# Kernel optimization log

Hardware: AMD Instinct MI355X
Metric: run time of the kernel (lower is better)

The kernel has to match this reference:

```python
import jax, jax.numpy as jnp
import numpy as np
import math

ROPE_BASE = 10000.0
ALIBI_SLOPE = 2.0 ** (-8.0)  # _get_alibi_slopes(1) == [2**(-8*1/1)]


def _rope_cos_sin(T, d):
    inv_freq = 1.0 / (ROPE_BASE ** (jnp.arange(0, d, 2, dtype=jnp.float32) / d))
    t = jnp.arange(T, dtype=jnp.float32)
    freqs = jnp.einsum('i,j->ij', t, inv_freq)          # [T, d/2]
    emb = jnp.concatenate([freqs, freqs], axis=-1)      # [T, d]
    return jnp.cos(emb), jnp.sin(emb)


def _rotate_half(x):
    x1, x2 = jnp.split(x, 2, axis=-1)
    return jnp.concatenate([-x2, x1], axis=-1)


def setup_inputs() -> dict:
    key = jax.random.key(0)
    kq, kk, kv = jax.random.split(key, 3)
    B, T, H = 8, 2048, 256
    return {
        'q': jax.random.normal(kq, (B, T, H), dtype=jnp.float32),
        'k': jax.random.normal(kk, (B, T, H), dtype=jnp.float32),
        'v': jax.random.normal(kv, (B, T, H), dtype=jnp.float32),
    }


def reference(q, k, v):
    B, T, H = q.shape  # num_heads == 1, so head_dim == H
    cos, sin = _rope_cos_sin(T, H)                      # [T, H]
    qe = q * cos + _rotate_half(q) * sin                # [B, T, H]
    ke = k * cos + _rotate_half(k) * sin                # [B, T, H]

    scale = 1.0 / math.sqrt(H)
    scores = jnp.einsum('btd,bsd->bts', qe, ke) * scale  # [B, T, T]

    pos = jnp.arange(T)
    rel = (pos[None, :] - pos[:, None]).astype(jnp.float32)  # [T, T]
    alibi = (ALIBI_SLOPE * rel)[None, None, :, :]            # [1, 1, T, T]

    # torch broadcast: [B,T,T] + [1,1,T,T] -> [1,B,T,T]
    scores = scores + alibi
    attn = jax.nn.softmax(scores, axis=-1)              # [1, B, T, T]
    out = jnp.matmul(attn, v)                           # [1, B, T, H]
    return out
```

## Files before the change

kernel.cpp:

```cpp
#include <hip/hip_runtime.h>

#define B_ 8
#define T_ 2048
#define H_ 256
#define PSTR 40
#define SCALE2 0.0901684403f
#define SLOPE2 0.00563552752f

typedef __attribute__((ext_vector_type(8))) short bf16x8;
typedef __attribute__((ext_vector_type(4))) float f32x4;

#define MFMA16(a, b, c) __builtin_amdgcn_mfma_f32_16x16x32_bf16((a), (b), (c), 0, 0, 0)

__device__ __forceinline__ ushort f2bf(float f) {
  unsigned u = __float_as_uint(f);
  u += 0x7FFFu + ((u >> 16) & 1u);
  return (ushort)(u >> 16);
}

__device__ __forceinline__ void gl_lds16(const ushort* g, ushort* l) {
  __builtin_amdgcn_global_load_lds(
      (const __attribute__((address_space(1))) unsigned int*)g,
      (__attribute__((address_space(3))) unsigned int*)l, 16, 0, 0);
}

__global__ void prep_kernel(const float* __restrict__ k, const float* __restrict__ v,
                            ushort* __restrict__ kt, ushort* __restrict__ vt) {
  __shared__ ushort tile[64][72];
  const int bid = blockIdx.x;
  const int tid = threadIdx.x;
  if (bid < 4096) {
    int idx = bid * 256 + tid;
    int jp = idx & 63, bt = idx >> 6;
    int t = bt & (T_ - 1);
    int b = bt >> 11;
    int j = jp * 2;
    float rv0 = (float)t * exp2f((float)j * -0.103810252959f) * 0.15915494309f;
    float rv1 = (float)t * exp2f((float)(j + 1) * -0.103810252959f) * 0.15915494309f;
    float fr0 = rv0 - floorf(rv0), fr1 = rv1 - floorf(rv1);
    float sn0 = __builtin_amdgcn_sinf(fr0), cs0 = __builtin_amdgcn_cosf(fr0);
    float sn1 = __builtin_amdgcn_sinf(fr1), cs1 = __builtin_amdgcn_cosf(fr1);
    size_t base = (size_t)bt * H_ + j;
    float2 a = *(const float2*)(k + base);
    float2 c = *(const float2*)(k + base + 128);
    ushort2 lo, hi;
    lo.x = f2bf(a.x * cs0 - c.x * sn0); lo.y = f2bf(a.y * cs1 - c.y * sn1);
    hi.x = f2bf(c.x * cs0 + a.x * sn0); hi.y = f2bf(c.y * cs1 + a.y * sn1);
    size_t kdst = (((size_t)(b * 64 + (t >> 5)) * 32 + (j >> 3)) * 32 + (t & 31)) * 8 + (j & 7);
    *(ushort2*)(kt + kdst) = lo;
    *(ushort2*)(kt + kdst + 4096) = hi;
  } else {
    int bid2 = bid - 4096;
    int b = bid2 >> 7, rem = bid2 & 127;
    int h0 = (rem >> 5) * 64, t0 = (rem & 31) * 64;
    int c4 = tid & 15, r0 = tid >> 4;
#pragma unroll
    for (int p = 0; p < 4; ++p) {
      int row = r0 + p * 16;
      const float4 f = *(const float4*)(v + ((size_t)(b * T_ + t0 + row)) * H_ + h0 + c4 * 4);
      ushort4 u;
      u.x = f2bf(f.x); u.y = f2bf(f.y); u.z = f2bf(f.z); u.w = f2bf(f.w);
      *(ushort4*)&tile[row][(c4 * 4) ^ (8 * ((row >> 3) & 7))] = u;
    }
    __syncthreads();
#pragma unroll
    for (int p = 0; p < 2; ++p) {
      int c = tid + p * 256;
      int h = c >> 3, tc = (c & 7) * 8;
      int xo = 8 * (c & 7);
      ushort4 u0, u1;
      u0.x = tile[tc + 0][h ^ xo]; u0.y = tile[tc + 1][h ^ xo];
      u0.z = tile[tc + 2][h ^ xo]; u0.w = tile[tc + 3][h ^ xo];
      u1.x = tile[tc + 4][h ^ xo]; u1.y = tile[tc + 5][h ^ xo];
      u1.z = tile[tc + 6][h ^ xo]; u1.w = tile[tc + 7][h ^ xo];
      int tg = t0 + tc;
      size_t dst = (((size_t)(b * 64 + (tg >> 5)) * 4 + ((tg >> 3) & 3)) * 256 + (h0 + h)) * 8;
      *(ushort4*)(vt + dst) = u0;
      *(ushort4*)(vt + dst + 4) = u1;
    }
  }
}

__global__ __launch_bounds__(128, 1)
void attn_kernel(const float* __restrict__ q, const ushort* __restrict__ kt,
                 const ushort* __restrict__ vt, float* __restrict__ out,
                 float* __restrict__ o1, float* __restrict__ lpart) {
  __shared__ ushort Ksh[2][8192];
  __shared__ ushort Vsh[8192];
  __shared__ ushort Psh[2][32 * PSTR];

  const int tid = threadIdx.x;
  const int w = tid >> 6, lane = tid & 63, quad = lane >> 4, l16 = lane & 15;
  const int b = blockIdx.x;
  const int q0 = blockIdx.y * 64;
  const int sp = blockIdx.z;
  const int kvb = sp * (T_ / 2);

  bf16x8 aq[2][8];
  {
    const float* qb = q + ((size_t)(b * T_) + q0 + w * 32) * H_;
#pragma unroll
    for (int mt = 0; mt < 2; ++mt) {
      int t = q0 + w * 32 + mt * 16 + l16;
      float qv[8][8];
#pragma unroll
      for (int ks = 0; ks < 8; ++ks) {
        float4 x0 = *(const float4*)(qb + (size_t)(mt * 16 + l16) * H_ + ks * 32 + quad * 8);
        float4 x1 = *(const float4*)(qb + (size_t)(mt * 16 + l16) * H_ + ks * 32 + quad * 8 + 4);
        qv[ks][0] = x0.x; qv[ks][1] = x0.y; qv[ks][2] = x0.z; qv[ks][3] = x0.w;
        qv[ks][4] = x1.x; qv[ks][5] = x1.y; qv[ks][6] = x1.z; qv[ks][7] = x1.w;
      }
#pragma unroll
      for (int ks = 0; ks < 4; ++ks)
#pragma unroll
        for (int e = 0; e < 8; ++e) {
          int d = ks * 32 + quad * 8 + e;
          float rv = (float)t * exp2f((float)d * -0.103810252959f) * 0.15915494309f;
          float fr = rv - floorf(rv);
          float sn = __builtin_amdgcn_sinf(fr), cs = __builtin_amdgcn_cosf(fr);
          aq[mt][ks][e]     = (short)f2bf(qv[ks][e] * cs - qv[ks + 4][e] * sn);
          aq[mt][ks + 4][e] = (short)f2bf(qv[ks + 4][e] * cs + qv[ks][e] * sn);
        }
    }
  }

  const f32x4 fzero = {0.f, 0.f, 0.f, 0.f};
  f32x4 O[2][16], lac[2];
#pragma unroll
  for (int mt = 0; mt < 2; ++mt) {
    lac[mt] = fzero;
#pragma unroll
    for (int ht = 0; ht < 16; ++ht) O[mt][ht] = fzero;
  }
  bf16x8 vones;
#pragma unroll
  for (int i = 0; i < 8; ++i) vones[i] = (short)0x3F80;

  const ushort* ktb = kt + (size_t)(b * 64 + sp * 32) * 8192;
  const ushort* vtb = vt + (size_t)(b * 64 + sp * 32) * 8192;
  const int stoff = w * 4096 + lane * 8;

#pragma unroll
  for (int i = 0; i < 8; ++i)
    gl_lds16(ktb + stoff + i * 512, &Ksh[0][stoff + i * 512]);
  __builtin_amdgcn_sched_barrier(0);
  __builtin_amdgcn_s_waitcnt(0x0070);
  __builtin_amdgcn_s_barrier();
  __builtin_amdgcn_sched_barrier(0);

  const float arb = SLOPE2 * (float)(q0 + w * 32 + quad * 4);

  for (int it = 0; it < 32; ++it) {
    const int p = it & 1;
    {
      const ushort* vg = vtb + (size_t)it * 8192;
#pragma unroll
      for (int i = 0; i < 8; ++i)
        gl_lds16(vg + stoff + i * 512, &Vsh[stoff + i * 512]);
      const int itn = (it < 31) ? it + 1 : 31;
      const ushort* kg = ktb + (size_t)itn * 8192;
#pragma unroll
      for (int i = 0; i < 8; ++i)
        gl_lds16(kg + stoff + i * 512, &Ksh[1 - p][stoff + i * 512]);
    }
    __builtin_amdgcn_sched_barrier(0);

    f32x4 s[2][2] = {{fzero, fzero}, {fzero, fzero}};
#pragma unroll
    for (int ks = 0; ks < 8; ++ks)
#pragma unroll
      for (int nt = 0; nt < 2; ++nt) {
        bf16x8 kf = *(const bf16x8*)&Ksh[p][((ks * 4 + quad) * 32 + nt * 16 + l16) * 8];
        s[0][nt] = MFMA16(aq[0][ks], kf, s[0][nt]);
        s[1][nt] = MFMA16(aq[1][ks], kf, s[1][nt]);
      }

    __builtin_amdgcn_sched_barrier(0);
    __builtin_amdgcn_s_waitcnt(0x0F78);
    __builtin_amdgcn_s_barrier();
    __builtin_amdgcn_sched_barrier(0);

#pragma unroll
    for (int nt = 0; nt < 2; ++nt) {
      float ac = SLOPE2 * (float)(kvb + it * 32 + nt * 16 + l16);
#pragma unroll
      for (int mt = 0; mt < 2; ++mt)
#pragma unroll
        for (int r = 0; r < 4; ++r) {
          float a0 = ac - arb - SLOPE2 * (float)(mt * 16 + r);
          float pv = __builtin_amdgcn_exp2f(fmaf(s[mt][nt][r], SCALE2, a0));
          Psh[w][(mt * 16 + quad * 4 + r) * PSTR + nt * 16 + l16] = f2bf(pv);
        }
    }

    bf16x8 pf0 = *(const bf16x8*)&Psh[w][l16 * PSTR + quad * 8];
    bf16x8 pf1 = *(const bf16x8*)&Psh[w][(16 + l16) * PSTR + quad * 8];
    lac[0] = MFMA16(pf0, vones, lac[0]);
    lac[1] = MFMA16(pf1, vones, lac[1]);
#pragma unroll
    for (int ht = 0; ht < 16; ++ht) {
      bf16x8 vf = *(const bf16x8*)&Vsh[(quad * 256 + ht * 16 + l16) * 8];
      O[0][ht] = MFMA16(pf0, vf, O[0][ht]);
      O[1][ht] = MFMA16(pf1, vf, O[1][ht]);
    }

    __builtin_amdgcn_sched_barrier(0);
    __builtin_amdgcn_s_waitcnt(0x0070);
    __builtin_amdgcn_s_barrier();
    __builtin_amdgcn_sched_barrier(0);
  }

  float* od = (sp == 0) ? out : o1;
  float* ob = od + ((size_t)(b * T_) + q0 + w * 32) * H_;
#pragma unroll
  for (int mt = 0; mt < 2; ++mt)
#pragma unroll
    for (int r = 0; r < 4; ++r) {
      int row = mt * 16 + quad * 4 + r;
#pragma unroll
      for (int ht = 0; ht < 16; ++ht)
        ob[(size_t)row * H_ + ht * 16 + l16] = O[mt][ht][r];
    }
  if (l16 == 0) {
#pragma unroll
    for (int mt = 0; mt < 2; ++mt)
#pragma unroll
      for (int r = 0; r < 4; ++r)
        lpart[(size_t)(sp * B_ + b) * T_ + q0 + w * 32 + mt * 16 + quad * 4 + r] =
            lac[mt][r];
  }
}

__global__ void combine_kernel(float* __restrict__ out, const float* __restrict__ o1,
                               const float* __restrict__ lpart) {
  int idx = blockIdx.x * 256 + threadIdx.x;
  int row = idx >> 6;
  float inv = 1.0f / (lpart[row] + lpart[B_ * T_ + row]);
  float4 a = ((const float4*)out)[idx];
  float4 c = ((const float4*)o1)[idx];
  a.x = (a.x + c.x) * inv; a.y = (a.y + c.y) * inv;
  a.z = (a.z + c.z) * inv; a.w = (a.w + c.w) * inv;
  ((float4*)out)[idx] = a;
}

extern "C" void kernel_launch(void* const* d_in, const int* in_sizes, int n_in,
                              void* d_out, int out_size, void* d_ws, size_t ws_size,
                              hipStream_t stream) {
  const float* q = (const float*)d_in[0];
  const float* k = (const float*)d_in[1];
  const float* v = (const float*)d_in[2];
  float* out = (float*)d_out;

  const size_t elems = (size_t)B_ * T_ * H_;
  ushort* kt = (ushort*)d_ws;
  ushort* vt = kt + elems;
  float* o1 = (float*)(vt + elems);
  float* lpart = o1 + elems;

  prep_kernel<<<dim3(5120), 256, 0, stream>>>(k, v, kt, vt);
  attn_kernel<<<dim3(B_, T_ / 64, 2), 128, 0, stream>>>(q, kt, vt, out, o1, lpart);
  combine_kernel<<<dim3((B_ * T_ * H_ / 4) / 256), 256, 0, stream>>>(out, o1, lpart);
}
```

Before: 165.1 us.

## Precompute rotated Q in prep kernel and double-buffer V tiles

Q's rotary embedding and bf16 conversion move from the attention kernel prologue into the prep kernel, which writes a bf16 Q buffer the attention kernel loads directly. The K rotation is reorganised so each thread handles 8 contiguous dims. V gets a second LDS buffer and is prefetched one iteration ahead together with K, which removes the mid-iteration wait and barrier that previously guarded the V load. This trades an extra global write/read of Q and doubled V LDS use for less prologue work and more load/compute overlap.

```diff
diff --git a/kernel.cpp b/kernel.cpp
--- a/kernel.cpp
+++ b/kernel.cpp
@@ -6,6 +6,8 @@
 #define PSTR 40
 #define SCALE2 0.0901684403f
 #define SLOPE2 0.00563552752f
+#define NFREQ 0.103810252959f
+#define INV2PI 0.15915494309f
 
 typedef __attribute__((ext_vector_type(8))) short bf16x8;
 typedef __attribute__((ext_vector_type(4))) float f32x4;
@@ -24,31 +26,59 @@
       (__attribute__((address_space(3))) unsigned int*)l, 16, 0, 0);
 }
 
-__global__ void prep_kernel(const float* __restrict__ k, const float* __restrict__ v,
+__global__ void prep_kernel(const float* __restrict__ q, const float* __restrict__ k,
+                            const float* __restrict__ v, ushort* __restrict__ qe,
                             ushort* __restrict__ kt, ushort* __restrict__ vt) {
   __shared__ ushort tile[64][72];
   const int bid = blockIdx.x;
   const int tid = threadIdx.x;
-  if (bid < 4096) {
+  if (bid < 2048) {
     int idx = bid * 256 + tid;
-    int jp = idx & 63, bt = idx >> 6;
+    int j = (idx & 31) * 4, bt = idx >> 5;
     int t = bt & (T_ - 1);
-    int b = bt >> 11;
-    int j = jp * 2;
-    float rv0 = (float)t * exp2f((float)j * -0.103810252959f) * 0.15915494309f;
-    float rv1 = (float)t * exp2f((float)(j + 1) * -0.103810252959f) * 0.15915494309f;
-    float fr0 = rv0 - floorf(rv0), fr1 = rv1 - floorf(rv1);
-    float sn0 = __builtin_amdgcn_sinf(fr0), cs0 = __builtin_amdgcn_cosf(fr0);
-    float sn1 = __builtin_amdgcn_sinf(fr1), cs1 = __builtin_amdgcn_cosf(fr1);
+    float cs[4], sn[4];
+#pragma unroll
+    for (int i = 0; i < 4; ++i) {
+      float rv = (float)t * exp2f((float)(j + i) * -NFREQ) * INV2PI;
+      float fr = rv - floorf(rv);
+      sn[i] = __builtin_amdgcn_sinf(fr);
+      cs[i] = __builtin_amdgcn_cosf(fr);
+    }
     size_t base = (size_t)bt * H_ + j;
-    float2 a = *(const float2*)(k + base);
-    float2 c = *(const float2*)(k + base + 128);
-    ushort2 lo, hi;
-    lo.x = f2bf(a.x * cs0 - c.x * sn0); lo.y = f2bf(a.y * cs1 - c.y * sn1);
-    hi.x = f2bf(c.x * cs0 + a.x * sn0); hi.y = f2bf(c.y * cs1 + a.y * sn1);
-    size_t kdst = (((size_t)(b * 64 + (t >> 5)) * 32 + (j >> 3)) * 32 + (t & 31)) * 8 + (j & 7);
-    *(ushort2*)(kt + kdst) = lo;
-    *(ushort2*)(kt + kdst + 4096) = hi;
+    float4 lo = *(const float4*)(q + base);
+    float4 hi = *(const float4*)(q + base + 128);
+    ushort4 olo, ohi;
+    olo.x = f2bf(lo.x * cs[0] - hi.x * sn[0]); ohi.x = f2bf(hi.x * cs[0] + lo.x * sn[0]);
+    olo.y = f2bf(lo.y * cs[1] - hi.y * sn[1]); ohi.y = f2bf(hi.y * cs[1] + lo.y * sn[1]);
+    olo.z = f2bf(lo.z * cs[2] - hi.z * sn[2]); ohi.z = f2bf(hi.z * cs[2] + lo.z * sn[2]);
+    olo.w = f2bf(lo.w * cs[3] - hi.w * sn[3]); ohi.w = f2bf(hi.w * cs[3] + lo.w * sn[3]);
+    *(ushort4*)(qe + base) = olo; *(ushort4*)(qe + base + 128) = ohi;
+  } else if (bid < 4096) {
+    int c = (bid - 2048) * 256 + tid;
+    int kv = c & 31, d8 = (c >> 5) & 31, itk = (c >> 10) & 63, b = c >> 16;
+    int t = itk * 32 + kv, d0 = d8 * 8;
+    const float* kr = k + ((size_t)(b * T_ + t)) * H_;
+    float4 a0 = *(const float4*)(kr + d0);
+    float4 a1 = *(const float4*)(kr + d0 + 4);
+    int hi = d0 >= 128;
+    int pd = hi ? d0 - 128 : d0 + 128;
+    float4 b0 = *(const float4*)(kr + pd);
+    float4 b1 = *(const float4*)(kr + pd + 4);
+    int j0 = d0 & 127;
+    float xs[8] = {a0.x, a0.y, a0.z, a0.w, a1.x, a1.y, a1.z, a1.w};
+    float ps[8] = {b0.x, b0.y, b0.z, b0.w, b1.x, b1.y, b1.z, b1.w};
+    ushort o[8];
+#pragma unroll
+    for (int i = 0; i < 8; ++i) {
+      float rv = (float)t * exp2f((float)(j0 + i) * -NFREQ) * INV2PI;
+      float fr = rv - floorf(rv);
+      float sn = __builtin_amdgcn_sinf(fr), cn = __builtin_amdgcn_cosf(fr);
+      o[i] = f2bf(hi ? (xs[i] * cn + ps[i] * sn) : (xs[i] * cn - ps[i] * sn));
+    }
+    size_t dst = ((((size_t)b * 64 + itk) * 32 + d8) * 32 + kv) * 8;
+    ushort4 w0 = {o[0], o[1], o[2], o[3]}, w1 = {o[4], o[5], o[6], o[7]};
+    *(ushort4*)(kt + dst) = w0;
+    *(ushort4*)(kt + dst + 4) = w1;
   } else {
     int bid2 = bid - 4096;
     int b = bid2 >> 7, rem = bid2 & 127;
@@ -82,11 +112,11 @@
 }
 
 __global__ __launch_bounds__(128, 1)
-void attn_kernel(const float* __restrict__ q, const ushort* __restrict__ kt,
+void attn_kernel(const ushort* __restrict__ qe, const ushort* __restrict__ kt,
                  const ushort* __restrict__ vt, float* __restrict__ out,
                  float* __restrict__ o1, float* __restrict__ lpart) {
   __shared__ ushort Ksh[2][8192];
-  __shared__ ushort Vsh[8192];
+  __shared__ ushort Vsh[2][8192];
   __shared__ ushort Psh[2][32 * PSTR];
 
   const int tid = threadIdx.x;
@@ -97,32 +127,12 @@
   const int kvb = sp * (T_ / 2);
 
   bf16x8 aq[2][8];
-  {
-    const float* qb = q + ((size_t)(b * T_) + q0 + w * 32) * H_;
-#pragma unroll
-    for (int mt = 0; mt < 2; ++mt) {
-      int t = q0 + w * 32 + mt * 16 + l16;
-      float qv[8][8];
-#pragma unroll
-      for (int ks = 0; ks < 8; ++ks) {
-        float4 x0 = *(const float4*)(qb + (size_t)(mt * 16 + l16) * H_ + ks * 32 + quad * 8);
-        float4 x1 = *(const float4*)(qb + (size_t)(mt * 16 + l16) * H_ + ks * 32 + quad * 8 + 4);
-        qv[ks][0] = x0.x; qv[ks][1] = x0.y; qv[ks][2] = x0.z; qv[ks][3] = x0.w;
-        qv[ks][4] = x1.x; qv[ks][5] = x1.y; qv[ks][6] = x1.z; qv[ks][7] = x1.w;
-      }
-#pragma unroll
-      for (int ks = 0; ks < 4; ++ks)
-#pragma unroll
-        for (int e = 0; e < 8; ++e) {
-          int d = ks * 32 + quad * 8 + e;
-          float rv = (float)t * exp2f((float)d * -0.103810252959f) * 0.15915494309f;
-          float fr = rv - floorf(rv);
-          float sn = __builtin_amdgcn_sinf(fr), cs = __builtin_amdgcn_cosf(fr);
-          aq[mt][ks][e]     = (short)f2bf(qv[ks][e] * cs - qv[ks + 4][e] * sn);
-          aq[mt][ks + 4][e] = (short)f2bf(qv[ks + 4][e] * cs + qv[ks][e] * sn);
-        }
-    }
-  }
+  const ushort* qb = qe + ((size_t)(b * T_) + q0 + w * 32) * H_;
+#pragma unroll
+  for (int mt = 0; mt < 2; ++mt)
+#pragma unroll
+    for (int ks = 0; ks < 8; ++ks)
+      aq[mt][ks] = *(const bf16x8*)(qb + (size_t)(mt * 16 + l16) * H_ + ks * 32 + quad * 8);
 
   const f32x4 fzero = {0.f, 0.f, 0.f, 0.f};
   f32x4 O[2][16], lac[2];
@@ -143,6 +153,9 @@
 #pragma unroll
   for (int i = 0; i < 8; ++i)
     gl_lds16(ktb + stoff + i * 512, &Ksh[0][stoff + i * 512]);
+#pragma unroll
+  for (int i = 0; i < 8; ++i)
+    gl_lds16(vtb + stoff + i * 512, &Vsh[0][stoff + i * 512]);
   __builtin_amdgcn_sched_barrier(0);
   __builtin_amdgcn_s_waitcnt(0x0070);
   __builtin_amdgcn_s_barrier();
@@ -152,16 +165,15 @@
 
   for (int it = 0; it < 32; ++it) {
     const int p = it & 1;
-    {
-      const ushort* vg = vtb + (size_t)it * 8192;
-#pragma unroll
-      for (int i = 0; i < 8; ++i)
-        gl_lds16(vg + stoff + i * 512, &Vsh[stoff + i * 512]);
-      const int itn = (it < 31) ? it + 1 : 31;
-      const ushort* kg = ktb + (size_t)itn * 8192;
+    if (it < 31) {
+      const ushort* kg = ktb + (size_t)(it + 1) * 8192;
+      const ushort* vg = vtb + (size_t)(it + 1) * 8192;
 #pragma unroll
       for (int i = 0; i < 8; ++i)
         gl_lds16(kg + stoff + i * 512, &Ksh[1 - p][stoff + i * 512]);
+#pragma unroll
+      for (int i = 0; i < 8; ++i)
+        gl_lds16(vg + stoff + i * 512, &Vsh[1 - p][stoff + i * 512]);
     }
     __builtin_amdgcn_sched_barrier(0);
 
@@ -175,11 +187,6 @@
         s[1][nt] = MFMA16(aq[1][ks], kf, s[1][nt]);
       }
 
-    __builtin_amdgcn_sched_barrier(0);
-    __builtin_amdgcn_s_waitcnt(0x0F78);
-    __builtin_amdgcn_s_barrier();
-    __builtin_amdgcn_sched_barrier(0);
-
 #pragma unroll
     for (int nt = 0; nt < 2; ++nt) {
       float ac = SLOPE2 * (float)(kvb + it * 32 + nt * 16 + l16);
@@ -199,7 +206,7 @@
     lac[1] = MFMA16(pf1, vones, lac[1]);
 #pragma unroll
     for (int ht = 0; ht < 16; ++ht) {
-      bf16x8 vf = *(const bf16x8*)&Vsh[(quad * 256 + ht * 16 + l16) * 8];
+      bf16x8 vf = *(const bf16x8*)&Vsh[p][(quad * 256 + ht * 16 + l16) * 8];
       O[0][ht] = MFMA16(pf0, vf, O[0][ht]);
       O[1][ht] = MFMA16(pf1, vf, O[1][ht]);
     }
@@ -252,12 +259,13 @@
   float* out = (float*)d_out;
 
   const size_t elems = (size_t)B_ * T_ * H_;
-  ushort* kt = (ushort*)d_ws;
+  ushort* qe = (ushort*)d_ws;
+  ushort* kt = qe + elems;
   ushort* vt = kt + elems;
   float* o1 = (float*)(vt + elems);
   float* lpart = o1 + elems;
 
-  prep_kernel<<<dim3(5120), 256, 0, stream>>>(k, v, kt, vt);
-  attn_kernel<<<dim3(B_, T_ / 64, 2), 128, 0, stream>>>(q, kt, vt, out, o1, lpart);
+  prep_kernel<<<dim3(5120), 256, 0, stream>>>(q, k, v, qe, kt, vt);
+  attn_kernel<<<dim3(B_, T_ / 64, 2), 128, 0, stream>>>(qe, kt, vt, out, o1, lpart);
   combine_kernel<<<dim3((B_ * T_ * H_ / 4) / 256), 256, 0, stream>>>(out, o1, lpart);
 }
```

Measured after the change: 173.6 us. 5.1% more time.
